# Kernel optimization log

Measured on AMD Instinct MI355X. Metric: run time of the kernel, lower is better.

## Reference

```python
import jax, jax.numpy as jnp
import numpy as np

B, N, DIM = 2, 2048, 1024
HEADS, DIM_HEAD = 8, 64
INNER = HEADS * DIM_HEAD  # 512
EPS = 1e-5  # fp32 branch of the source LayerNorm


def setup_inputs() -> dict:
    key = jax.random.key(0)
    ks = jax.random.split(key, 5)
    x = jax.random.normal(ks[0], (B, N, DIM), dtype=jnp.float32)
    g = jnp.ones((DIM,), dtype=jnp.float32)  # LayerNorm gain init
    # Linear weights stored as (in, out) so y = x @ W. Source zero-inits
    # to_out; we use small random values so the baseline output is nonzero.
    wq = jax.random.normal(ks[1], (DIM, INNER), dtype=jnp.float32) * 0.02
    wkv = jax.random.normal(ks[2], (DIM, 2 * INNER), dtype=jnp.float32) * 0.02
    wo = jax.random.normal(ks[3], (INNER, DIM), dtype=jnp.float32) * 0.02
    return {"x": x, "g": g, "wq": wq, "wkv": wkv, "wo": wo}


def reference(x, g, wq, wkv, wo):
    # Custom LayerNorm from the source: statistics over dim=1 (sequence axis!)
    mean = jnp.mean(x, axis=1, keepdims=True)
    var = jnp.var(x, axis=1, keepdims=True)  # unbiased=False
    xn = (x - mean) * jax.lax.rsqrt(var + EPS) * g  # g broadcasts on last dim

    q = xn @ wq                      # [b, n, inner]
    kv = xn @ wkv                    # [b, n, 2*inner]
    k, v = jnp.split(kv, 2, axis=-1)

    def split_heads(t):  # b n (h d) -> b h n d
        b, n, _ = t.shape
        return t.reshape(b, n, HEADS, DIM_HEAD).transpose(0, 2, 1, 3)

    q, k, v = map(split_heads, (q, k, v))
    q = q * (DIM_HEAD ** -0.5)

    sim = jnp.einsum('bhid,bhjd->bhij', q, k)   # [b, h, n, n]
    attn = jax.nn.softmax(sim, axis=-1)
    out = jnp.einsum('bhij,bhjd->bhid', attn, v)  # [b, h, n, d]

    out = out.transpose(0, 2, 1, 3).reshape(B, N, INNER)  # b h n d -> b n (h d)
    return out @ wo  # [b, n, dim]
```

## Files before the change

kernel.cpp:

```cpp
#include <hip/hip_runtime.h>
#include <hip/hip_bf16.h>
#include <stdint.h>


#define B_ 2
#define N_ 2048
#define DIM_ 1024
#define DH_ 64
#define INNER_ 512
#define ROWS_ 4096
#define BHSTRIDE 131072

#define QSCALE 0.18033688011112042f

typedef __bf16 bf16x8 __attribute__((ext_vector_type(8)));
typedef float floatx4 __attribute__((ext_vector_type(4)));

#if __has_builtin(__builtin_amdgcn_exp2f)
#define EXP2(x) __builtin_amdgcn_exp2f(x)
#else
#define EXP2(x) exp2f(x)
#endif

__device__ __forceinline__ ushort f2bf(float f) {
    union { float f; uint32_t u; } v; v.f = f;
    uint32_t u = v.u;
    u += 0x7fffu + ((u >> 16) & 1u);
    return (ushort)(u >> 16);
}
__device__ __forceinline__ uint32_t pkbf(float a, float b) {
    return (uint32_t)f2bf(a) | ((uint32_t)f2bf(b) << 16);
}
__device__ __forceinline__ size_t frag_off(int m, int k, int nkc) {
    return ((size_t)((m >> 4) * nkc + (k >> 5)) * 64 +
            (size_t)((m & 15) | (((k >> 3) & 3) << 4))) * 8 + (k & 7);
}

__global__ __launch_bounds__(256) void setup_fused(
    const float* __restrict__ x, float* __restrict__ ps, float* __restrict__ pq,
    const float* __restrict__ wq, const float* __restrict__ wkv,
    const float* __restrict__ wo, ushort* __restrict__ wqkv_f,
    ushort* __restrict__ wo_f) {
    __shared__ float tile[32][33];
    int bid = blockIdx.x;
    if (bid < 256) {
        int gd = (bid & 7) * 256 + threadIdx.x;
        int ch = bid >> 3;
        int b = gd >> 10;
        const float* p = x + (size_t)(b * N_ + ch * 64) * DIM_ + (gd & 1023);
        float s = 0.f, q = 0.f;
#pragma unroll 4
        for (int n = 0; n < 64; ++n) { float v = p[(size_t)n * DIM_]; s += v; q += v * v; }
        ps[ch * 2048 + gd] = s;
        pq[ch * 2048 + gd] = q;
        return;
    }
    int t = bid - 256;
    const float* src; ushort* dst; int C, K, k0, ncol0, nglob0; float scale;
    if (t < 512) {
        int kt = t >> 4, nt = t & 15;
        src = wq; dst = wqkv_f; C = 512; K = 1024; scale = QSCALE;
        k0 = kt * 32; ncol0 = nt * 32; nglob0 = ncol0;
    } else if (t < 1536) {
        int u = t - 512; int kt = u >> 5, nt = u & 31;
        src = wkv; dst = wqkv_f; C = 1024; K = 1024; scale = 1.f;
        k0 = kt * 32; ncol0 = nt * 32; nglob0 = 512 + ncol0;
    } else {
        int u = t - 1536; int kt = u >> 5, nt = u & 31;
        src = wo; dst = wo_f; C = 1024; K = 512; scale = 1.f;
        k0 = kt * 32; ncol0 = nt * 32; nglob0 = ncol0;
    }
    int ti = threadIdx.x >> 5, tj = threadIdx.x & 31;
#pragma unroll
    for (int p = 0; p < 4; ++p)
        tile[ti + 8 * p][tj] = src[(size_t)(k0 + ti + 8 * p) * C + ncol0 + tj] * scale;
    __syncthreads();
    if (threadIdx.x < 128) {
        int nl = threadIdx.x & 31, kc8 = threadIdx.x >> 5;
        union { ushort us[8]; uint4 v; } u;
#pragma unroll
        for (int ii = 0; ii < 8; ++ii) u.us[ii] = f2bf(tile[kc8 * 8 + ii][nl]);
        *(uint4*)&dst[frag_off(nglob0 + nl, k0 + kc8 * 8, K >> 5)] = u.v;
    }
}

__global__ __launch_bounds__(256) void finalize_norm(
    const float* __restrict__ ps, const float* __restrict__ pq,
    const float* __restrict__ x, const float* __restrict__ g,
    ushort* __restrict__ xnf) {
    __shared__ float s4[4][64], q4[4][64], aa[64], bb[64];
    int t = threadIdx.x;
    int b = blockIdx.x >> 8, slab = (blockIdx.x >> 4) & 15, nch = blockIdx.x & 15;
    int c0 = slab * 64;
    {
        int c = t & 63, grp = t >> 6;
        float s = 0.f, q = 0.f;
#pragma unroll
        for (int ch = 0; ch < 8; ++ch) {
            int o = (grp * 8 + ch) * 2048 + b * 1024 + c0 + c;
            s += ps[o]; q += pq[o];
        }
        s4[grp][c] = s; q4[grp][c] = q;
    }
    __syncthreads();
    if (t < 64) {
        float s = s4[0][t] + s4[1][t] + s4[2][t] + s4[3][t];
        float q = q4[0][t] + q4[1][t] + q4[2][t] + q4[3][t];
        float mean = s * (1.f / N_);
        float var = q * (1.f / N_) - mean * mean;
        float rstd = rsqrtf(var + 1e-5f);
        float a = rstd * g[c0 + t];
        aa[t] = a; bb[t] = -mean * a;
    }
    __syncthreads();
    int c4 = (t & 15) * 4, ro = t >> 4;
#pragma unroll
    for (int it = 0; it < 8; ++it) {
        int r = nch * 128 + it * 16 + ro;
        int m = b * 2048 + r;
        float4 xv = *(const float4*)&x[(size_t)m * DIM_ + c0 + c4];
        float v0 = xv.x * aa[c4 + 0] + bb[c4 + 0];
        float v1 = xv.y * aa[c4 + 1] + bb[c4 + 1];
        float v2 = xv.z * aa[c4 + 2] + bb[c4 + 2];
        float v3 = xv.w * aa[c4 + 3] + bb[c4 + 3];
        uint2 u; u.x = pkbf(v0, v1); u.y = pkbf(v2, v3);
        *(uint2*)&xnf[frag_off(m, c0 + c4, 32)] = u;
    }
}

template <int NKC>
__device__ __forceinline__ void gemm_core(
    const ushort* __restrict__ pA, const ushort* __restrict__ pB,
    floatx4 (&acc)[4][4]) {
    constexpr int TS = NKC * 512;
    bf16x8 a0[4], b0[4], a1[4], b1[4];
#pragma unroll
    for (int i = 0; i < 4; ++i) {
        a0[i] = *(const bf16x8*)(pA + (size_t)i * TS);
        b0[i] = *(const bf16x8*)(pB + (size_t)i * TS);
    }
    for (int kc = 0; kc < NKC; kc += 2) {
#pragma unroll
        for (int i = 0; i < 4; ++i) {
            a1[i] = *(const bf16x8*)(pA + (size_t)i * TS + (size_t)(kc + 1) * 512);
            b1[i] = *(const bf16x8*)(pB + (size_t)i * TS + (size_t)(kc + 1) * 512);
        }
#pragma unroll
        for (int mi = 0; mi < 4; ++mi)
#pragma unroll
            for (int ni = 0; ni < 4; ++ni)
                acc[mi][ni] = __builtin_amdgcn_mfma_f32_16x16x32_bf16(
                    a0[mi], b0[ni], acc[mi][ni], 0, 0, 0);
        if (kc + 2 < NKC) {
#pragma unroll
            for (int i = 0; i < 4; ++i) {
                a0[i] = *(const bf16x8*)(pA + (size_t)i * TS + (size_t)(kc + 2) * 512);
                b0[i] = *(const bf16x8*)(pB + (size_t)i * TS + (size_t)(kc + 2) * 512);
            }
        }
#pragma unroll
        for (int mi = 0; mi < 4; ++mi)
#pragma unroll
            for (int ni = 0; ni < 4; ++ni)
                acc[mi][ni] = __builtin_amdgcn_mfma_f32_16x16x32_bf16(
                    a1[mi], b1[ni], acc[mi][ni], 0, 0, 0);
    }
}

__global__ __launch_bounds__(128) void gemm_qkv(
    const ushort* __restrict__ xnf, const ushort* __restrict__ wf,
    ushort* __restrict__ qf, ushort* __restrict__ kf, ushort* __restrict__ vf) {
    int tx = threadIdx.x, w = tx >> 6, l = tx & 63;
    int lr = l & 15, lq = l >> 4;
    int bid = blockIdx.x;
    int xcd = bid & 7, t = bid >> 3;
    int bx = xcd * 8 + (t & 7);
    int by = t >> 3;
    const ushort* pA = xnf + (size_t)(bx * 4) * 32 * 512 + l * 8;
    const ushort* pB = wf + (size_t)(by * 8 + w * 4) * 32 * 512 + l * 8;
    floatx4 acc[4][4] = {};
    gemm_core<32>(pA, pB, acc);
    int col0 = by * 128 + w * 64;
    int bb2 = (bx * 64) >> 11;
    if (by < 8) {
        ushort* qkbase = (by < 4) ? qf : kf;
#pragma unroll
        for (int ni = 0; ni < 4; ++ni) {
            int col = col0 + 16 * ni + lr;
            int hh = (col >> 6) & 7, d = col & 63;
            ushort* base = qkbase + (size_t)(bb2 * 8 + hh) * BHSTRIDE
                           + (d >> 5) * 512 + ((d >> 3) & 3) * 128 + (d & 7)
                           + (4 * lq) * 8;
#pragma unroll
            for (int mi = 0; mi < 4; ++mi) {
                size_t o2 = (size_t)((bx * 4 + mi) & 127) * 1024;
#pragma unroll
                for (int reg = 0; reg < 4; ++reg)
                    base[o2 + reg * 8] = f2bf(acc[mi][ni][reg]);
            }
        }
    } else {
#pragma unroll
        for (int ni = 0; ni < 4; ++ni) {
            int cv = col0 - 1024 + 16 * ni + lr;
            int hh = cv >> 6, d = cv & 63;
            ushort* base = vf + (size_t)(bb2 * 8 + hh) * BHSTRIDE
                           + (d >> 4) * 32768 + (d & 15) * 8;
#pragma unroll
            for (int mi = 0; mi < 4; ++mi) {
                int nn = (bx * 64 + 16 * mi + 4 * lq) & 2047;
                uint2 u;
                u.x = pkbf(acc[mi][ni][0], acc[mi][ni][1]);
                u.y = pkbf(acc[mi][ni][2], acc[mi][ni][3]);
                *(uint2*)&base[(nn >> 5) * 512 + ((nn >> 3) & 3) * 128 + (nn & 7)] = u;
            }
        }
    }
}

__global__ __launch_bounds__(128) void gemm_out(
    const ushort* __restrict__ af, const ushort* __restrict__ wf,
    float* __restrict__ out) {
    int tx = threadIdx.x, w = tx >> 6, l = tx & 63;
    int lr = l & 15, lq = l >> 4;
    int bid = blockIdx.x;
    int xcd = bid & 7, t = bid >> 3;
    int bx = xcd * 8 + (t & 7);
    int by = t >> 3;
    const ushort* pA = af + (size_t)(bx * 4) * 16 * 512 + l * 8;
    const ushort* pB = wf + (size_t)(by * 8 + w * 4) * 16 * 512 + l * 8;
    floatx4 acc[4][4] = {};
    gemm_core<16>(pA, pB, acc);
    int col0 = by * 128 + w * 64;
#pragma unroll
    for (int mi = 0; mi < 4; ++mi)
#pragma unroll
        for (int ni = 0; ni < 4; ++ni) {
            int col = col0 + 16 * ni + lr;
#pragma unroll
            for (int reg = 0; reg < 4; ++reg) {
                int row = bx * 64 + 16 * mi + 4 * lq + reg;
                out[(size_t)row * 1024 + col] = acc[mi][ni][reg];
            }
        }
}

__global__ __launch_bounds__(256, 2) void flash_attn(
    const ushort* __restrict__ qf, const ushort* __restrict__ kf,
    const ushort* __restrict__ vf, ushort* __restrict__ attnf) {
    __shared__ __align__(16) float sArena[4 * 4352];
    __shared__ float sL[4][64];

    const int tx = threadIdx.x;
    const int w = tx >> 6, l = tx & 63;
    const int lr = l & 15, lq = l >> 4;
    const int bid = blockIdx.x;
    const int bh = (bid & 7) * 2 + ((bid >> 3) & 1);
    const int qt = bid >> 4;

    const ushort* qfb = qf + (size_t)bh * BHSTRIDE + (size_t)(qt * 4) * 1024 + l * 8;
    const ushort* kfb = kf + (size_t)bh * BHSTRIDE + (size_t)w * 32768 + l * 8;
    const ushort* vfb = vf + (size_t)bh * BHSTRIDE + (size_t)w * 8192 + l * 8;
    ushort* sPw = (ushort*)(sArena + w * 4352);

    bf16x8 bq[4][2];
#pragma unroll
    for (int qq = 0; qq < 4; ++qq)
#pragma unroll
        for (int s = 0; s < 2; ++s)
            bq[qq][s] = *(const bf16x8*)(qfb + qq * 1024 + s * 512);

    floatx4 o[4][4] = {};
    float lsum[4] = {0.f, 0.f, 0.f, 0.f};

    bf16x8 ak[8], bv[8];
#pragma unroll
    for (int kk = 0; kk < 4; ++kk) {
        ak[kk * 2 + 0] = *(const bf16x8*)(kfb + kk * 1024);
        ak[kk * 2 + 1] = *(const bf16x8*)(kfb + kk * 1024 + 512);
    }

    for (int kt = 0; kt < 8; ++kt) {
#pragma unroll
        for (int dt = 0; dt < 4; ++dt) {
            bv[dt * 2 + 0] = *(const bf16x8*)(vfb + dt * 32768 + (kt * 2 + 0) * 512);
            bv[dt * 2 + 1] = *(const bf16x8*)(vfb + dt * 32768 + (kt * 2 + 1) * 512);
        }

        floatx4 c[4][4] = {};
#pragma unroll
        for (int s = 0; s < 2; ++s)
#pragma unroll
            for (int kk = 0; kk < 4; ++kk)
#pragma unroll
                for (int qq = 0; qq < 4; ++qq)
                    c[kk][qq] = __builtin_amdgcn_mfma_f32_16x16x32_bf16(
                        ak[kk * 2 + s], bq[qq][s], c[kk][qq], 0, 0, 0);

        if (kt + 1 < 8) {
            const ushort* kp = kfb + (size_t)(kt + 1) * 4096;
#pragma unroll
            for (int kk = 0; kk < 4; ++kk) {
                ak[kk * 2 + 0] = *(const bf16x8*)(kp + kk * 1024);
                ak[kk * 2 + 1] = *(const bf16x8*)(kp + kk * 1024 + 512);
            }
        }

#pragma unroll
        for (int kk = 0; kk < 4; ++kk)
#pragma unroll
            for (int qq = 0; qq < 4; ++qq) {
                float e0 = EXP2(c[kk][qq][0]);
                float e1 = EXP2(c[kk][qq][1]);
                float e2 = EXP2(c[kk][qq][2]);
                float e3 = EXP2(c[kk][qq][3]);
                lsum[qq] += (e0 + e1) + (e2 + e3);
                uint2 u; u.x = pkbf(e0, e1); u.y = pkbf(e2, e3);
                *(uint2*)&sPw[(16 * qq + lr) * 72 + 16 * kk + 4 * lq] = u;
            }

#pragma unroll
        for (int s = 0; s < 2; ++s) {
            bf16x8 ap[4];
#pragma unroll
            for (int mi = 0; mi < 4; ++mi)
                ap[mi] = *(const bf16x8*)&sPw[(16 * mi + lr) * 72 + 32 * s + 8 * lq];
#pragma unroll
            for (int mi = 0; mi < 4; ++mi)
#pragma unroll
                for (int dt = 0; dt < 4; ++dt)
                    o[mi][dt] = __builtin_amdgcn_mfma_f32_16x16x32_bf16(
                        ap[mi], bv[dt * 2 + s], o[mi][dt], 0, 0, 0);
        }
    }

#pragma unroll
    for (int qq = 0; qq < 4; ++qq) {
        lsum[qq] += __shfl_xor(lsum[qq], 16);
        lsum[qq] += __shfl_xor(lsum[qq], 32);
    }

    float* Rw = sArena + w * 4352;
#pragma unroll
    for (int mi = 0; mi < 4; ++mi)
#pragma unroll
        for (int dt = 0; dt < 4; ++dt)
#pragma unroll
            for (int reg = 0; reg < 4; ++reg)
                Rw[(16 * mi + 4 * lq + reg) * 68 + 16 * dt + lr] = o[mi][dt][reg];
    if (lq == 0) {
#pragma unroll
        for (int qq = 0; qq < 4; ++qq) sL[w][16 * qq + lr] = lsum[qq];
    }
    __syncthreads();

    int qloc = 16 * w + (l >> 2);
    int c0 = (l & 3) * 16;
    float4 acc[4];
#pragma unroll
    for (int rg = 0; rg < 4; ++rg) {
        const float* R = sArena + rg * 4352 + qloc * 68 + c0;
#pragma unroll
        for (int c = 0; c < 4; ++c) {
            float4 v = *(const float4*)&R[4 * c];
            if (rg == 0) acc[c] = v;
            else { acc[c].x += v.x; acc[c].y += v.y; acc[c].z += v.z; acc[c].w += v.w; }
        }
    }
    float ltot = sL[0][qloc] + sL[1][qloc] + sL[2][qloc] + sL[3][qloc];
    float inv = 1.f / ltot;
    int m = (bh >> 3) * 2048 + qt * 64 + qloc;
    int kb = (bh & 7) * 64 + c0;
#pragma unroll
    for (int c = 0; c < 4; ++c) {
        uint2 u;
        u.x = pkbf(acc[c].x * inv, acc[c].y * inv);
        u.y = pkbf(acc[c].z * inv, acc[c].w * inv);
        *(uint2*)&attnf[frag_off(m, kb + 4 * c, 16)] = u;
    }
}

extern "C" void kernel_launch(void* const* d_in, const int* in_sizes, int n_in,
                              void* d_out, int out_size, void* d_ws, size_t ws_size,
                              hipStream_t stream) {
    const float* x   = (const float*)d_in[0];
    const float* g   = (const float*)d_in[1];
    const float* wq  = (const float*)d_in[2];
    const float* wkv = (const float*)d_in[3];
    const float* wo  = (const float*)d_in[4];
    float* out = (float*)d_out;

    char* ws = (char*)d_ws;
    float*  psum   = (float*)(ws + 0);
    float*  psqr   = (float*)(ws + 262144);
    ushort* xnf    = (ushort*)(ws + 524288);
    ushort* wqkv_f = (ushort*)(ws + 8912896);
    ushort* wo_f   = (ushort*)(ws + 12058624);
    ushort* qfb    = (ushort*)(ws + 13107200);
    ushort* kfb    = (ushort*)(ws + 17301504);
    ushort* vfb    = (ushort*)(ws + 21495808);
    ushort* attnf  = (ushort*)(ws + 25690112);

    setup_fused<<<2304, 256, 0, stream>>>(x, psum, psqr, wq, wkv, wo, wqkv_f, wo_f);
    finalize_norm<<<512, 256, 0, stream>>>(psum, psqr, x, g, xnf);
    gemm_qkv<<<768, 128, 0, stream>>>(xnf, wqkv_f, qfb, kfb, vfb);
    flash_attn<<<512, 256, 0, stream>>>(qfb, kfb, vfb, attnf);
    gemm_out<<<512, 128, 0, stream>>>(attnf, wo_f, out);
}
```

Baseline: 147.3 us.

## Triple-buffer GEMM loads, shrink out-GEMM tiles, split attention QK/softmax for register pressure

```diff
diff --git a/kernel.cpp b/kernel.cpp
--- a/kernel.cpp
+++ b/kernel.cpp
@@ -129,45 +129,75 @@
 }
 
 template <int NKC>
-__device__ __forceinline__ void gemm_core(
+__device__ __forceinline__ void gemm_core3(
     const ushort* __restrict__ pA, const ushort* __restrict__ pB,
     floatx4 (&acc)[4][4]) {
     constexpr int TS = NKC * 512;
-    bf16x8 a0[4], b0[4], a1[4], b1[4];
-#pragma unroll
-    for (int i = 0; i < 4; ++i) {
-        a0[i] = *(const bf16x8*)(pA + (size_t)i * TS);
-        b0[i] = *(const bf16x8*)(pB + (size_t)i * TS);
-    }
-    for (int kc = 0; kc < NKC; kc += 2) {
+    bf16x8 a[3][4], b[3][4];
+#pragma unroll
+    for (int st = 0; st < 2; ++st)
 #pragma unroll
         for (int i = 0; i < 4; ++i) {
-            a1[i] = *(const bf16x8*)(pA + (size_t)i * TS + (size_t)(kc + 1) * 512);
-            b1[i] = *(const bf16x8*)(pB + (size_t)i * TS + (size_t)(kc + 1) * 512);
+            a[st][i] = *(const bf16x8*)(pA + (size_t)i * TS + (size_t)st * 512);
+            b[st][i] = *(const bf16x8*)(pB + (size_t)i * TS + (size_t)st * 512);
+        }
+#pragma unroll
+    for (int kc = 0; kc < NKC; ++kc) {
+        const int cur = kc % 3;
+        const int nxt = (kc + 2) % 3;
+        if (kc + 2 < NKC) {
+#pragma unroll
+            for (int i = 0; i < 4; ++i) {
+                a[nxt][i] = *(const bf16x8*)(pA + (size_t)i * TS + (size_t)(kc + 2) * 512);
+                b[nxt][i] = *(const bf16x8*)(pB + (size_t)i * TS + (size_t)(kc + 2) * 512);
+            }
         }
 #pragma unroll
         for (int mi = 0; mi < 4; ++mi)
 #pragma unroll
             for (int ni = 0; ni < 4; ++ni)
                 acc[mi][ni] = __builtin_amdgcn_mfma_f32_16x16x32_bf16(
-                    a0[mi], b0[ni], acc[mi][ni], 0, 0, 0);
+                    a[cur][mi], b[cur][ni], acc[mi][ni], 0, 0, 0);
+    }
+}
+
+template <int NKC>
+__device__ __forceinline__ void gemm_core3_24(
+    const ushort* __restrict__ pA, const ushort* __restrict__ pB,
+    floatx4 (&acc)[2][4]) {
+    constexpr int TS = NKC * 512;
+    bf16x8 a[3][2], b[3][4];
+#pragma unroll
+    for (int st = 0; st < 2; ++st) {
+#pragma unroll
+        for (int i = 0; i < 2; ++i)
+            a[st][i] = *(const bf16x8*)(pA + (size_t)i * TS + (size_t)st * 512);
+#pragma unroll
+        for (int i = 0; i < 4; ++i)
+            b[st][i] = *(const bf16x8*)(pB + (size_t)i * TS + (size_t)st * 512);
+    }
+#pragma unroll
+    for (int kc = 0; kc < NKC; ++kc) {
+        const int cur = kc % 3;
+        const int nxt = (kc + 2) % 3;
         if (kc + 2 < NKC) {
 #pragma unroll
-            for (int i = 0; i < 4; ++i) {
-                a0[i] = *(const bf16x8*)(pA + (size_t)i * TS + (size_t)(kc + 2) * 512);
-                b0[i] = *(const bf16x8*)(pB + (size_t)i * TS + (size_t)(kc + 2) * 512);
-            }
-        }
-#pragma unroll
-        for (int mi = 0; mi < 4; ++mi)
+            for (int i = 0; i < 2; ++i)
+                a[nxt][i] = *(const bf16x8*)(pA + (size_t)i * TS + (size_t)(kc + 2) * 512);
+#pragma unroll
+            for (int i = 0; i < 4; ++i)
+                b[nxt][i] = *(const bf16x8*)(pB + (size_t)i * TS + (size_t)(kc + 2) * 512);
+        }
+#pragma unroll
+        for (int mi = 0; mi < 2; ++mi)
 #pragma unroll
             for (int ni = 0; ni < 4; ++ni)
                 acc[mi][ni] = __builtin_amdgcn_mfma_f32_16x16x32_bf16(
-                    a1[mi], b1[ni], acc[mi][ni], 0, 0, 0);
-    }
-}
-
-__global__ __launch_bounds__(128) void gemm_qkv(
+                    a[cur][mi], b[cur][ni], acc[mi][ni], 0, 0, 0);
+    }
+}
+
+__global__ __launch_bounds__(128, 2) void gemm_qkv(
     const ushort* __restrict__ xnf, const ushort* __restrict__ wf,
     ushort* __restrict__ qf, ushort* __restrict__ kf, ushort* __restrict__ vf) {
     int tx = threadIdx.x, w = tx >> 6, l = tx & 63;
@@ -179,7 +209,7 @@
     const ushort* pA = xnf + (size_t)(bx * 4) * 32 * 512 + l * 8;
     const ushort* pB = wf + (size_t)(by * 8 + w * 4) * 32 * 512 + l * 8;
     floatx4 acc[4][4] = {};
-    gemm_core<32>(pA, pB, acc);
+    gemm_core3<32>(pA, pB, acc);
     int col0 = by * 128 + w * 64;
     int bb2 = (bx * 64) >> 11;
     if (by < 8) {
@@ -218,28 +248,27 @@
     }
 }
 
-__global__ __launch_bounds__(128) void gemm_out(
+__global__ __launch_bounds__(128, 2) void gemm_out(
     const ushort* __restrict__ af, const ushort* __restrict__ wf,
     float* __restrict__ out) {
     int tx = threadIdx.x, w = tx >> 6, l = tx & 63;
     int lr = l & 15, lq = l >> 4;
     int bid = blockIdx.x;
     int xcd = bid & 7, t = bid >> 3;
-    int bx = xcd * 8 + (t & 7);
-    int by = t >> 3;
-    const ushort* pA = af + (size_t)(bx * 4) * 16 * 512 + l * 8;
-    const ushort* pB = wf + (size_t)(by * 8 + w * 4) * 16 * 512 + l * 8;
-    floatx4 acc[4][4] = {};
-    gemm_core<16>(pA, pB, acc);
-    int col0 = by * 128 + w * 64;
-#pragma unroll
-    for (int mi = 0; mi < 4; ++mi)
+    int mt = xcd * 16 + (t & 15);
+    int nt = (t >> 4) * 2 + w;
+    const ushort* pA = af + (size_t)(mt * 2) * 16 * 512 + l * 8;
+    const ushort* pB = wf + (size_t)(nt * 4) * 16 * 512 + l * 8;
+    floatx4 acc[2][4] = {};
+    gemm_core3_24<16>(pA, pB, acc);
+#pragma unroll
+    for (int mi = 0; mi < 2; ++mi)
 #pragma unroll
         for (int ni = 0; ni < 4; ++ni) {
-            int col = col0 + 16 * ni + lr;
+            int col = nt * 64 + 16 * ni + lr;
 #pragma unroll
             for (int reg = 0; reg < 4; ++reg) {
-                int row = bx * 64 + 16 * mi + 4 * lq + reg;
+                int row = mt * 32 + 16 * mi + 4 * lq + reg;
                 out[(size_t)row * 1024 + col] = acc[mi][ni][reg];
             }
         }
@@ -273,7 +302,7 @@
     floatx4 o[4][4] = {};
     float lsum[4] = {0.f, 0.f, 0.f, 0.f};
 
-    bf16x8 ak[8], bv[8];
+    bf16x8 ak[8];
 #pragma unroll
     for (int kk = 0; kk < 4; ++kk) {
         ak[kk * 2 + 0] = *(const bf16x8*)(kfb + kk * 1024);
@@ -281,21 +310,58 @@
     }
 
     for (int kt = 0; kt < 8; ++kt) {
-#pragma unroll
-        for (int dt = 0; dt < 4; ++dt) {
-            bv[dt * 2 + 0] = *(const bf16x8*)(vfb + dt * 32768 + (kt * 2 + 0) * 512);
-            bv[dt * 2 + 1] = *(const bf16x8*)(vfb + dt * 32768 + (kt * 2 + 1) * 512);
-        }
-
-        floatx4 c[4][4] = {};
+        floatx4 c2[2][4] = {};
 #pragma unroll
         for (int s = 0; s < 2; ++s)
 #pragma unroll
-            for (int kk = 0; kk < 4; ++kk)
+            for (int kk = 0; kk < 2; ++kk)
 #pragma unroll
                 for (int qq = 0; qq < 4; ++qq)
-                    c[kk][qq] = __builtin_amdgcn_mfma_f32_16x16x32_bf16(
-                        ak[kk * 2 + s], bq[qq][s], c[kk][qq], 0, 0, 0);
+                    c2[kk][qq] = __builtin_amdgcn_mfma_f32_16x16x32_bf16(
+                        ak[kk * 2 + s], bq[qq][s], c2[kk][qq], 0, 0, 0);
+#pragma unroll
+        for (int kk = 0; kk < 2; ++kk)
+#pragma unroll
+            for (int qq = 0; qq < 4; ++qq) {
+                float e0 = EXP2(c2[kk][qq][0]);
+                float e1 = EXP2(c2[kk][qq][1]);
+                float e2 = EXP2(c2[kk][qq][2]);
+                float e3 = EXP2(c2[kk][qq][3]);
+                lsum[qq] += (e0 + e1) + (e2 + e3);
+                uint2 u; u.x = pkbf(e0, e1); u.y = pkbf(e2, e3);
+                *(uint2*)&sPw[(16 * qq + lr) * 72 + 16 * kk + 4 * lq] = u;
+            }
+
+#pragma unroll
+        for (int kk = 0; kk < 2; ++kk)
+#pragma unroll
+            for (int qq = 0; qq < 4; ++qq) c2[kk][qq] = floatx4{0.f, 0.f, 0.f, 0.f};
+#pragma unroll
+        for (int s = 0; s < 2; ++s)
+#pragma unroll
+            for (int kk = 0; kk < 2; ++kk)
+#pragma unroll
+                for (int qq = 0; qq < 4; ++qq)
+                    c2[kk][qq] = __builtin_amdgcn_mfma_f32_16x16x32_bf16(
+                        ak[(kk + 2) * 2 + s], bq[qq][s], c2[kk][qq], 0, 0, 0);
+
+        bf16x8 bv0[4];
+#pragma unroll
+        for (int dt = 0; dt < 4; ++dt)
+            bv0[dt] = *(const bf16x8*)(vfb + dt * 32768 + (size_t)(kt * 2 + 0) * 512);
+
+#pragma unroll
+        for (int kk = 0; kk < 2; ++kk)
+#pragma unroll
+            for (int qq = 0; qq < 4; ++qq) {
+                float e0 = EXP2(c2[kk][qq][0]);
+                float e1 = EXP2(c2[kk][qq][1]);
+                float e2 = EXP2(c2[kk][qq][2]);
+                float e3 = EXP2(c2[kk][qq][3]);
+                lsum[qq] += (e0 + e1) + (e2 + e3);
+                uint2 u; u.x = pkbf(e0, e1); u.y = pkbf(e2, e3);
+                *(uint2*)&sPw[(16 * qq + lr) * 72 + 16 * (kk + 2) + 4 * lq] = u;
+            }
 
         if (kt + 1 < 8) {
             const ushort* kp = kfb + (size_t)(kt + 1) * 4096;
@@ -306,31 +372,33 @@
             }
         }
 
-#pragma unroll
-        for (int kk = 0; kk < 4; ++kk)
-#pragma unroll
-            for (int qq = 0; qq < 4; ++qq) {
-                float e0 = EXP2(c[kk][qq][0]);
-                float e1 = EXP2(c[kk][qq][1]);
-                float e2 = EXP2(c[kk][qq][2]);
-                float e3 = EXP2(c[kk][qq][3]);
-                lsum[qq] += (e0 + e1) + (e2 + e3);
-                uint2 u; u.x = pkbf(e0, e1); u.y = pkbf(e2, e3);
-                *(uint2*)&sPw[(16 * qq + lr) * 72 + 16 * kk + 4 * lq] = u;
-            }
-
-#pragma unroll
-        for (int s = 0; s < 2; ++s) {
+        {
             bf16x8 ap[4];
 #pragma unroll
             for (int mi = 0; mi < 4; ++mi)
-                ap[mi] = *(const bf16x8*)&sPw[(16 * mi + lr) * 72 + 32 * s + 8 * lq];
+                ap[mi] = *(const bf16x8*)&sPw[(16 * mi + lr) * 72 + 8 * lq];
 #pragma unroll
             for (int mi = 0; mi < 4; ++mi)
 #pragma unroll
                 for (int dt = 0; dt < 4; ++dt)
                     o[mi][dt] = __builtin_amdgcn_mfma_f32_16x16x32_bf16(
-                        ap[mi], bv[dt * 2 + s], o[mi][dt], 0, 0, 0);
+                        ap[mi], bv0[dt], o[mi][dt], 0, 0, 0);
+        }
+        {
+            bf16x8 bv1[4];
+#pragma unroll
+            for (int dt = 0; dt < 4; ++dt)
+                bv1[dt] = *(const bf16x8*)(vfb + dt * 32768 + (size_t)(kt * 2 + 1) * 512);
+            bf16x8 ap[4];
+#pragma unroll
+            for (int mi = 0; mi < 4; ++mi)
+                ap[mi] = *(const bf16x8*)&sPw[(16 * mi + lr) * 72 + 32 + 8 * lq];
+#pragma unroll
+            for (int mi = 0; mi < 4; ++mi)
+#pragma unroll
+                for (int dt = 0; dt < 4; ++dt)
+                    o[mi][dt] = __builtin_amdgcn_mfma_f32_16x16x32_bf16(
+                        ap[mi], bv1[dt], o[mi][dt], 0, 0, 0);
         }
     }
 
@@ -405,5 +473,5 @@
     finalize_norm<<<512, 256, 0, stream>>>(psum, psqr, x, g, xnf);
     gemm_qkv<<<768, 128, 0, stream>>>(xnf, wqkv_f, qfb, kfb, vfb);
     flash_attn<<<512, 256, 0, stream>>>(qfb, kfb, vfb, attnf);
-    gemm_out<<<512, 128, 0, stream>>>(attnf, wo_f, out);
-}
+    gemm_out<<<1024, 128, 0, stream>>>(attnf, wo_f, out);
+}
```

Result: slower. 180.8 us (+22.7%).
